# Kernel optimization log

Measured on AMD Instinct MI355X. Metric: run time of the kernel, lower is better.

The kernel has to match this reference:

```python
import jax, jax.numpy as jnp
import numpy as np

N = 100000
E = 3200000
NFEAT = 256
NHID = 128
NCLASS = 16
TEXT_CNT = 50000


def setup_inputs() -> dict:
    key = jax.random.key(0)
    ks = jax.random.split(key, 12)
    x = jax.random.normal(ks[0], (N, NFEAT), dtype=jnp.float32)
    adj_rows = jax.random.randint(ks[1], (E,), 0, N, dtype=jnp.int32)
    adj_cols = jax.random.randint(ks[2], (E,), 0, N, dtype=jnp.int32)
    # positive normalized-adjacency-like weights (~1/avg_degree scale)
    adj_vals = jax.random.uniform(ks[3], (E,), dtype=jnp.float32) / 32.0
    W1 = jax.random.normal(ks[4], (NFEAT, NHID), dtype=jnp.float32) / np.sqrt(NFEAT)
    b1 = jax.random.normal(ks[5], (NHID,), dtype=jnp.float32) * 0.01
    W2 = jax.random.normal(ks[6], (NHID, NFEAT), dtype=jnp.float32) / np.sqrt(NHID)
    b2 = jax.random.normal(ks[7], (NFEAT,), dtype=jnp.float32) * 0.01
    cW1 = jax.random.normal(ks[8], (NFEAT, NCLASS), dtype=jnp.float32) / np.sqrt(NFEAT)
    cb1 = jax.random.normal(ks[9], (NCLASS,), dtype=jnp.float32) * 0.01
    cW2 = jax.random.normal(ks[10], (NFEAT, NCLASS), dtype=jnp.float32) / np.sqrt(NFEAT)
    cb2 = jax.random.normal(ks[11], (NCLASS,), dtype=jnp.float32) * 0.01
    return {"x": x, "adj_rows": adj_rows, "adj_cols": adj_cols, "adj_vals": adj_vals,
            "W1": W1, "b1": b1, "W2": W2, "b2": b2,
            "cW1": cW1, "cb1": cb1, "cW2": cw2 if (cw2 := None) else cW2, "cb2": cb2}


def spmm(rows, cols, vals, dense):
    # out[r] = sum_{e: rows[e]==r} vals[e] * dense[cols[e]]   (COO SpMM)
    gathered = vals[:, None] * dense[cols]  # [E, D]
    return jax.ops.segment_sum(gathered, rows, num_segments=N)


def reference(x, adj_rows, adj_cols, adj_vals, W1, b1, W2, b2, cW1, cb1, cW2, cb2):
    # gc1: adj @ (x @ W1) + b1, then ReLU (dropout is identity at inference)
    h = jax.nn.relu(spmm(adj_rows, adj_cols, adj_vals, x @ W1) + b1)  # [N, NHID]
    # gc2: adj @ (h @ W2) + b2
    out = spmm(adj_rows, adj_cols, adj_vals, h @ W2) + b2  # [N, NFEAT]
    text_cls = out[:TEXT_CNT] @ cW1 + cb1  # [TEXT_CNT, NCLASS]
    img_cls = out[TEXT_CNT:] @ cW2 + cb2   # [N-TEXT_CNT, NCLASS]
    return (out, text_cls, img_cls)
```

## Files before the change

kernel.cpp:

```cpp
#include <hip/hip_runtime.h>

#define N_NODES  100000
#define N_EDGES  3200000
#define NFEAT    256
#define NHID     128
#define NCLASS   16
#define TEXT_CNT 50000

#define RPB      256
#define NB       ((N_NODES + RPB - 1) / RPB)
#define CAP      16384
#define S_EPT    32

typedef unsigned int uint;
typedef __bf16 bf16x8 __attribute__((ext_vector_type(8)));
typedef __bf16 bf16x4 __attribute__((ext_vector_type(4)));
typedef float f32x4 __attribute__((ext_vector_type(4)));

__device__ inline uint bf16_rne(float f) {
  uint u = __float_as_uint(f);
  return (u + 0x7fffu + ((u >> 16) & 1u)) >> 16;
}
__device__ inline float bf_lo(uint u) { return __uint_as_float(u << 16); }
__device__ inline float bf_hi(uint u) { return __uint_as_float(u & 0xffff0000u); }


__global__ __launch_bounds__(256) void init_cursor_kernel(int* __restrict__ gcursor) {
  int t = blockIdx.x * 256 + threadIdx.x;
  if (t < NB) gcursor[t] = t * CAP;
}


__global__ __launch_bounds__(256) void bucket_scatter_kernel(const int* __restrict__ rows,
                                                             const int* __restrict__ cols,
                                                             const float* __restrict__ vals,
                                                             int* __restrict__ gcursor,
                                                             int2* __restrict__ packed, int E) {
  __shared__ int hist[NB];
  __shared__ int cur[NB];
  for (int i = threadIdx.x; i < NB; i += 256) hist[i] = 0;
  __syncthreads();
  int base = blockIdx.x * (256 * S_EPT);
#pragma unroll
  for (int i = 0; i < S_EPT; ++i) {
    int e = base + i * 256 + threadIdx.x;
    if (e < E) atomicAdd(&hist[rows[e] >> 8], 1);
  }
  __syncthreads();
  for (int i = threadIdx.x; i < NB; i += 256) {
    int h = hist[i];
    cur[i] = h ? atomicAdd(&gcursor[i], h) : 0;
  }
  __syncthreads();
#pragma unroll
  for (int i = 0; i < S_EPT; ++i) {
    int e = base + i * 256 + threadIdx.x;
    if (e < E) {
      int r = rows[e];
      int b = r >> 8;
      int p = atomicAdd(&cur[b], 1);
      if (p < ((b + 1) << 14))
        packed[p] = make_int2(((r & 255) << 17) | cols[e], __float_as_int(vals[e]));
    }
  }
}


__global__ __launch_bounds__(512) void bucket_scan_kernel(const int* __restrict__ gcursor,
                                                          int* __restrict__ bbase) {
  __shared__ int s[512];
  int t = threadIdx.x;
  int v = (t < NB) ? (gcursor[t] - t * CAP) : 0;
  s[t] = v;
  __syncthreads();
  for (int off = 1; off < 512; off <<= 1) {
    int u = (t >= off) ? s[t - off] : 0;
    __syncthreads();
    s[t] += u;
    __syncthreads();
  }
  if (t < NB) bbase[t] = s[t] - v;
  if (t == 0) bbase[NB] = N_EDGES;
}


__global__ __launch_bounds__(256) void csr_finalize_kernel(const int* __restrict__ bbase,
                                                           const int2* __restrict__ packed_in,
                                                           int2* __restrict__ packed_out,
                                                           int* __restrict__ row_ptr) {
  __shared__ int hist[RPB];
  __shared__ int cur[RPB];
  int b = blockIdx.x;
  int s0 = b * CAP;
  int gout = bbase[b];
  int cnt = bbase[b + 1] - gout;
  int end = s0 + cnt;
  int t = threadIdx.x;
  hist[t] = 0;
  __syncthreads();
  {
    int i = s0 + t;
    for (; i + 768 < end; i += 1024) {
      int2 a0 = packed_in[i], a1 = packed_in[i + 256];
      int2 a2 = packed_in[i + 512], a3 = packed_in[i + 768];
      atomicAdd(&hist[a0.x >> 17], 1);
      atomicAdd(&hist[a1.x >> 17], 1);
      atomicAdd(&hist[a2.x >> 17], 1);
      atomicAdd(&hist[a3.x >> 17], 1);
    }
    for (; i < end; i += 256) atomicAdd(&hist[packed_in[i].x >> 17], 1);
  }
  __syncthreads();
  int v = hist[t];
  cur[t] = v;
  __syncthreads();
  for (int off = 1; off < 256; off <<= 1) {
    int u = (t >= off) ? cur[t - off] : 0;
    __syncthreads();
    cur[t] += u;
    __syncthreads();
  }
  int rbase = gout + cur[t] - v;
  int row = b * RPB + t;
  if (row < N_NODES) row_ptr[row] = rbase;
  if (b == 0 && t == 0) row_ptr[N_NODES] = N_EDGES;
  __syncthreads();
  cur[t] = rbase;
  __syncthreads();
  {
    int i = s0 + t;
    for (; i + 768 < end; i += 1024) {
      int2 a0 = packed_in[i], a1 = packed_in[i + 256];
      int2 a2 = packed_in[i + 512], a3 = packed_in[i + 768];
      int p0 = atomicAdd(&cur[a0.x >> 17], 1);
      int p1 = atomicAdd(&cur[a1.x >> 17], 1);
      int p2 = atomicAdd(&cur[a2.x >> 17], 1);
      int p3 = atomicAdd(&cur[a3.x >> 17], 1);
      packed_out[p0] = make_int2((a0.x & 0x1FFFF) << 8, a0.y);
      packed_out[p1] = make_int2((a1.x & 0x1FFFF) << 8, a1.y);
      packed_out[p2] = make_int2((a2.x & 0x1FFFF) << 8, a2.y);
      packed_out[p3] = make_int2((a3.x & 0x1FFFF) << 8, a3.y);
    }
    for (; i < end; i += 256) {
      int2 pk = packed_in[i];
      int p = atomicAdd(&cur[pk.x >> 17], 1);
      packed_out[p] = make_int2((pk.x & 0x1FFFF) << 8, pk.y);
    }
  }
}


__global__ __launch_bounds__(256) void spmm_bf16_kernel(const int* __restrict__ row_ptr,
                                                        const int2* __restrict__ packed,
                                                        const uint* __restrict__ src,
                                                        uint* __restrict__ dst,
                                                        const float* __restrict__ bias,
                                                        int relu, int nrows) {
  int lane = threadIdx.x & 63;
  int row = blockIdx.x * 4 + (threadIdx.x >> 6);
  if (row >= nrows) return;
  int s = row_ptr[row];
  int e = row_ptr[row + 1];
  const char* srcb = (const char*)src + (lane << 2);
  float a0 = 0.f, a1 = 0.f;
  int i = s;
  for (; i + 8 <= e; i += 8) {
    int2 p0 = packed[i + 0], p1 = packed[i + 1], p2 = packed[i + 2], p3 = packed[i + 3];
    int2 p4 = packed[i + 4], p5 = packed[i + 5], p6 = packed[i + 6], p7 = packed[i + 7];
    uint u0 = *(const uint*)(srcb + (uint)p0.x);
    uint u1 = *(const uint*)(srcb + (uint)p1.x);
    uint u2 = *(const uint*)(srcb + (uint)p2.x);
    uint u3 = *(const uint*)(srcb + (uint)p3.x);
    uint u4 = *(const uint*)(srcb + (uint)p4.x);
    uint u5 = *(const uint*)(srcb + (uint)p5.x);
    uint u6 = *(const uint*)(srcb + (uint)p6.x);
    uint u7 = *(const uint*)(srcb + (uint)p7.x);
    float v0 = __int_as_float(p0.y), v1 = __int_as_float(p1.y);
    float v2 = __int_as_float(p2.y), v3 = __int_as_float(p3.y);
    float v4 = __int_as_float(p4.y), v5 = __int_as_float(p5.y);
    float v6 = __int_as_float(p6.y), v7 = __int_as_float(p7.y);
    a0 += v0 * bf_lo(u0); a1 += v0 * bf_hi(u0);
    a0 += v1 * bf_lo(u1); a1 += v1 * bf_hi(u1);
    a0 += v2 * bf_lo(u2); a1 += v2 * bf_hi(u2);
    a0 += v3 * bf_lo(u3); a1 += v3 * bf_hi(u3);
    a0 += v4 * bf_lo(u4); a1 += v4 * bf_hi(u4);
    a0 += v5 * bf_lo(u5); a1 += v5 * bf_hi(u5);
    a0 += v6 * bf_lo(u6); a1 += v6 * bf_hi(u6);
    a0 += v7 * bf_lo(u7); a1 += v7 * bf_hi(u7);
  }
  for (; i < e; ++i) {
    int2 pk = packed[i];
    float v = __int_as_float(pk.y);
    uint u = *(const uint*)(srcb + (uint)pk.x);
    a0 += v * bf_lo(u); a1 += v * bf_hi(u);
  }
  if (bias) { a0 += bias[2 * lane]; a1 += bias[2 * lane + 1]; }
  if (relu) { a0 = fmaxf(a0, 0.f); a1 = fmaxf(a1, 0.f); }
  dst[(size_t)row * 64 + lane] = bf16_rne(a0) | (bf16_rne(a1) << 16);
}


__global__ __launch_bounds__(256) void wt_kernel(const float* __restrict__ W,
                                                 unsigned short* __restrict__ Wt,
                                                 int K, int N) {
  int idx = blockIdx.x * 256 + threadIdx.x;
  if (idx >= K * N) return;
  int n = idx / K, k = idx - n * K;
  Wt[idx] = (unsigned short)bf16_rne(W[(size_t)k * N + n]);
}


template <int A_FP32, int OUT_BF16, int K, int N>
__global__ __launch_bounds__(256) void gemm_mfma_kernel(const void* __restrict__ Aptr,
                                                        const __bf16* __restrict__ Bt,
                                                        const float* __restrict__ bias,
                                                        void* __restrict__ Cptr, int M) {
  __shared__ __bf16 As[128 * 40];
  __shared__ __bf16 Bs[128 * 40];
  int tid = threadIdx.x;
  int lane = tid & 63;
  int w = tid >> 6;
  int wr = w >> 1, wc = w & 1;
  int brow = blockIdx.x * 128;
  int bcol = blockIdx.y * 128;
  int r16 = lane & 15, kb = lane >> 4;

  f32x4 acc[4][4];
#pragma unroll
  for (int m = 0; m < 4; ++m)
#pragma unroll
    for (int n = 0; n < 4; ++n) acc[m][n] = (f32x4){0.f, 0.f, 0.f, 0.f};

  for (int k0 = 0; k0 < K; k0 += 32) {
    if (A_FP32) {
      const float* A = (const float*)Aptr;
#pragma unroll
      for (int i = 0; i < 4; ++i) {
        int idx = tid + i * 256;
        int row = idx >> 3;
        int kq = (idx & 7) << 2;
        int gr = brow + row;
        float4 v = make_float4(0.f, 0.f, 0.f, 0.f);
        if (gr < M) v = *(const float4*)&A[(size_t)gr * K + k0 + kq];
        bf16x4 o;
        o[0] = (__bf16)v.x; o[1] = (__bf16)v.y; o[2] = (__bf16)v.z; o[3] = (__bf16)v.w;
        *(bf16x4*)&As[row * 40 + kq] = o;
      }
    } else {
      const __bf16* A = (const __bf16*)Aptr;
#pragma unroll
      for (int i = 0; i < 2; ++i) {
        int idx = tid + i * 256;
        int row = idx >> 2;
        int kq = (idx & 3) << 3;
        int gr = brow + row;
        bf16x8 v = {};
        if (gr < M) v = *(const bf16x8*)&A[(size_t)gr * K + k0 + kq];
        *(bf16x8*)&As[row * 40 + kq] = v;
      }
    }
#pragma unroll
    for (int i = 0; i < 2; ++i) {
      int idx = tid + i * 256;
      int col = idx >> 2;
      int kq = (idx & 3) << 3;
      bf16x8 v = *(const bf16x8*)&Bt[(size_t)(bcol + col) * K + k0 + kq];
      *(bf16x8*)&Bs[col * 40 + kq] = v;
    }
    __syncthreads();

    bf16x8 a[4], b[4];
#pragma unroll
    for (int m = 0; m < 4; ++m)
      a[m] = *(bf16x8*)&As[(wr * 64 + m * 16 + r16) * 40 + kb * 8];
#pragma unroll
    for (int n = 0; n < 4; ++n)
      b[n] = *(bf16x8*)&Bs[(wc * 64 + n * 16 + r16) * 40 + kb * 8];
#pragma unroll
    for (int m = 0; m < 4; ++m)
#pragma unroll
      for (int n = 0; n < 4; ++n)
        acc[m][n] = __builtin_amdgcn_mfma_f32_16x16x32_bf16(a[m], b[n], acc[m][n], 0, 0, 0);
    __syncthreads();
  }

  int crow0 = brow + wr * 64;
  int ccol0 = bcol + wc * 64;
#pragma unroll
  for (int n = 0; n < 4; ++n) {
    int col = ccol0 + n * 16 + r16;
    float bv = bias ? bias[col] : 0.f;
#pragma unroll
    for (int m = 0; m < 4; ++m) {
#pragma unroll
      for (int r = 0; r < 4; ++r) {
        int row = crow0 + m * 16 + kb * 4 + r;
        if (row < M) {
          float val = acc[m][n][r] + bv;
          if (OUT_BF16)
            ((unsigned short*)Cptr)[(size_t)row * N + col] = (unsigned short)bf16_rne(val);
          else
            ((float*)Cptr)[(size_t)row * N + col] = val;
        }
      }
    }
  }
}


__global__ __launch_bounds__(256) void wc_kernel(const float* __restrict__ W2,
                                                 const float* __restrict__ b2,
                                                 const float* __restrict__ cW1,
                                                 const float* __restrict__ cb1,
                                                 const float* __restrict__ cW2,
                                                 const float* __restrict__ cb2,
                                                 float* __restrict__ Wc1, float* __restrict__ bc1,
                                                 float* __restrict__ Wc2, float* __restrict__ bc2) {
  int idx = blockIdx.x * 256 + threadIdx.x;
  int set = idx >> 11;
  int e = idx & 2047;
  int i = e >> 4;
  int c = e & 15;
  const float* cw = set ? cW2 : cW1;
  float acc = 0.f;
  for (int k = 0; k < NFEAT; ++k)
    acc += W2[(size_t)i * NFEAT + k] * cw[k * NCLASS + c];
  (set ? Wc2 : Wc1)[e] = acc;
  if (idx < 32) {
    int s2 = idx >> 4, c2 = idx & 15;
    const float* cwb = s2 ? cW2 : cW1;
    float b = (s2 ? cb2 : cb1)[c2];
    for (int k = 0; k < NFEAT; ++k) b += b2[k] * cwb[k * NCLASS + c2];
    (s2 ? bc2 : bc1)[c2] = b;
  }
}


__global__ __launch_bounds__(256) void cls_kernel(const uint* __restrict__ t3,
                                                  const float* __restrict__ Wc1,
                                                  const float* __restrict__ bc1,
                                                  const float* __restrict__ Wc2,
                                                  const float* __restrict__ bc2,
                                                  float* __restrict__ out1,
                                                  float* __restrict__ out2) {
  int half = gridDim.x >> 1;
  int region = blockIdx.x >= half;
  int bid = region ? blockIdx.x - half : blockIdx.x;
  const float* Wc = region ? Wc2 : Wc1;
  const float* bc = region ? bc2 : bc1;
  float* outp = region ? out2 : out1;
  int row0 = region ? TEXT_CNT : 0;
  int nrows = region ? (N_NODES - TEXT_CNT) : TEXT_CNT;

  int lane = threadIdx.x & 63;
  int wav = bid * 4 + (threadIdx.x >> 6);
  int nw = half * 4;
  int c = lane & 15;
  int kg = lane >> 4;
  float w[32];
#pragma unroll
  for (int j = 0; j < 32; ++j) w[j] = Wc[(kg * 32 + j) * NCLASS + c];
  float bcv = bc[c];
  for (int r = wav; r < nrows; r += nw) {
    const uint4* rp = (const uint4*)&t3[(size_t)(row0 + r) * 64 + kg * 16];
    float acc = 0.f;
#pragma unroll
    for (int q = 0; q < 4; ++q) {
      uint4 u = rp[q];
      acc += bf_lo(u.x) * w[q * 8 + 0] + bf_hi(u.x) * w[q * 8 + 1]
           + bf_lo(u.y) * w[q * 8 + 2] + bf_hi(u.y) * w[q * 8 + 3]
           + bf_lo(u.z) * w[q * 8 + 4] + bf_hi(u.z) * w[q * 8 + 5]
           + bf_lo(u.w) * w[q * 8 + 6] + bf_hi(u.w) * w[q * 8 + 7];
    }
    acc += __shfl_xor(acc, 16);
    acc += __shfl_xor(acc, 32);
    if (lane < 16) outp[(size_t)r * NCLASS + lane] = acc + bcv;
  }
}


extern "C" void kernel_launch(void* const* d_in, const int* in_sizes, int n_in,
                              void* d_out, int out_size, void* d_ws, size_t ws_size,
                              hipStream_t stream) {
  const float* x     = (const float*)d_in[0];
  const int*   arows = (const int*)d_in[1];
  const int*   acols = (const int*)d_in[2];
  const float* avals = (const float*)d_in[3];
  const float* W1    = (const float*)d_in[4];
  const float* b1    = (const float*)d_in[5];
  const float* W2    = (const float*)d_in[6];
  const float* b2    = (const float*)d_in[7];
  const float* cW1   = (const float*)d_in[8];
  const float* cb1   = (const float*)d_in[9];
  const float* cW2   = (const float*)d_in[10];
  const float* cb2   = (const float*)d_in[11];
  float* outp = (float*)d_out;

  char* ws = (char*)d_ws;
  size_t off = 0;
  auto alloc = [&](size_t bytes) -> void* {
    void* p = ws + off;
    off += (bytes + 255) & ~(size_t)255;
    return p;
  };
  uint*  t1u     = (uint*) alloc((size_t)N_NODES * 64 * 4);
  uint*  hu      = (uint*) alloc((size_t)N_NODES * 64 * 4);
  uint*  t3u     = (uint*) alloc((size_t)N_NODES * 64 * 4);
  int2*  packedA = (int2*) alloc((size_t)NB * CAP * 8);
  int2*  packedB = (int2*) alloc((size_t)N_EDGES * 8);
  int*   bbase   = (int*)  alloc((size_t)(NB + 1) * 4);
  int*   gcursor = (int*)  alloc((size_t)NB * 4);
  int*   rowp    = (int*)  alloc((size_t)(N_NODES + 1) * 4);
  unsigned short* W1t = (unsigned short*)alloc((size_t)NHID * NFEAT * 2);
  unsigned short* W2t = (unsigned short*)alloc((size_t)NFEAT * NHID * 2);
  float* Wc1     = (float*)alloc(NHID * NCLASS * 4);
  float* Wc2     = (float*)alloc(NHID * NCLASS * 4);
  float* bc1     = (float*)alloc(64);
  float* bc2     = (float*)alloc(64);

  init_cursor_kernel<<<(NB + 255) / 256, 256, 0, stream>>>(gcursor);
  int nblkS = (N_EDGES + 256 * S_EPT - 1) / (256 * S_EPT);
  bucket_scatter_kernel<<<nblkS, 256, 0, stream>>>(arows, acols, avals, gcursor, packedA, N_EDGES);
  bucket_scan_kernel<<<1, 512, 0, stream>>>(gcursor, bbase);
  csr_finalize_kernel<<<NB, 256, 0, stream>>>(bbase, packedA, packedB, rowp);

  wt_kernel<<<(NFEAT * NHID + 255) / 256, 256, 0, stream>>>(W1, W1t, NFEAT, NHID);
  wt_kernel<<<(NFEAT * NHID + 255) / 256, 256, 0, stream>>>(W2, W2t, NHID, NFEAT);
  wc_kernel<<<16, 256, 0, stream>>>(W2, b2, cW1, cb1, cW2, cb2, Wc1, bc1, Wc2, bc2);

  int mblk = (N_NODES + 127) / 128;
  gemm_mfma_kernel<1, 1, NFEAT, NHID><<<dim3(mblk, 1), 256, 0, stream>>>(
      x, (const __bf16*)W1t, nullptr, t1u, N_NODES);
  spmm_bf16_kernel<<<(N_NODES + 3) / 4, 256, 0, stream>>>(rowp, packedB, t1u, hu, b1, 1, N_NODES);
  spmm_bf16_kernel<<<(N_NODES + 3) / 4, 256, 0, stream>>>(rowp, packedB, hu, t3u, nullptr, 0, N_NODES);
  gemm_mfma_kernel<0, 0, NHID, NFEAT><<<dim3(mblk, 2), 256, 0, stream>>>(
      t3u, (const __bf16*)W2t, b2, outp, N_NODES);
  cls_kernel<<<2048, 256, 0, stream>>>(t3u, Wc1, bc1, Wc2, bc2,
      outp + (size_t)N_NODES * NFEAT,
      outp + (size_t)N_NODES * NFEAT + (size_t)TEXT_CNT * NCLASS);
}
```

Measured before the change: 491.8 us.

## Fuse prep kernels, co-schedule scatter with GEMM1, widen SpMM gathers

Result: faster. 465.3 us (-5.4%).

```diff
diff --git a/kernel.cpp b/kernel.cpp
--- a/kernel.cpp
+++ b/kernel.cpp
@@ -10,7 +10,8 @@
 #define RPB      256
 #define NB       ((N_NODES + RPB - 1) / RPB)
 #define CAP      16384
-#define S_EPT    32
+#define S_EPT    8
+#define NBLKS    ((N_EDGES + 256 * S_EPT - 1) / (256 * S_EPT))
 
 typedef unsigned int uint;
 typedef __bf16 bf16x8 __attribute__((ext_vector_type(8)));
@@ -25,22 +26,60 @@
 __device__ inline float bf_hi(uint u) { return __uint_as_float(u & 0xffff0000u); }
 
 
-__global__ __launch_bounds__(256) void init_cursor_kernel(int* __restrict__ gcursor) {
-  int t = blockIdx.x * 256 + threadIdx.x;
-  if (t < NB) gcursor[t] = t * CAP;
-}
-
-
-__global__ __launch_bounds__(256) void bucket_scatter_kernel(const int* __restrict__ rows,
-                                                             const int* __restrict__ cols,
-                                                             const float* __restrict__ vals,
-                                                             int* __restrict__ gcursor,
-                                                             int2* __restrict__ packed, int E) {
+__global__ __launch_bounds__(256) void prep_kernel(const float* __restrict__ W1,
+                                                   const float* __restrict__ W2,
+                                                   const float* __restrict__ b2,
+                                                   const float* __restrict__ cW1,
+                                                   const float* __restrict__ cb1,
+                                                   const float* __restrict__ cW2,
+                                                   const float* __restrict__ cb2,
+                                                   unsigned short* __restrict__ W1t,
+                                                   unsigned short* __restrict__ W2t,
+                                                   float* __restrict__ Wc1, float* __restrict__ bc1,
+                                                   float* __restrict__ Wc2, float* __restrict__ bc2,
+                                                   int* __restrict__ gcursor) {
+  int idx = blockIdx.x * 256 + threadIdx.x;
+  if (idx < 32768) {
+    int n = idx >> 8, k = idx & 255;
+    W1t[idx] = (unsigned short)bf16_rne(W1[(size_t)k * NHID + n]);
+  } else if (idx < 65536) {
+    int i2 = idx - 32768;
+    int n = i2 >> 7, k = i2 & 127;
+    W2t[i2] = (unsigned short)bf16_rne(W2[(size_t)k * NFEAT + n]);
+  } else if (idx < 69632) {
+    int e = idx - 65536;
+    int set = e >> 11;
+    int e2 = e & 2047;
+    int i = e2 >> 4, c = e2 & 15;
+    const float* cw = set ? cW2 : cW1;
+    float acc = 0.f;
+    for (int k = 0; k < NFEAT; ++k)
+      acc += W2[(size_t)i * NFEAT + k] * cw[k * NCLASS + c];
+    (set ? Wc2 : Wc1)[e2] = acc;
+    if (e < 32) {
+      int s2 = e >> 4, c2 = e & 15;
+      const float* cwb = s2 ? cW2 : cW1;
+      float b = (s2 ? cb2 : cb1)[c2];
+      for (int k = 0; k < NFEAT; ++k) b += b2[k] * cwb[k * NCLASS + c2];
+      (s2 ? bc2 : bc1)[c2] = b;
+    }
+  } else if (idx < 69632 + NB) {
+    int b = idx - 69632;
+    gcursor[b] = b * CAP;
+  }
+}
+
+
+__device__ __forceinline__ void scatter_body(int bx, const int* __restrict__ rows,
+                                             const int* __restrict__ cols,
+                                             const float* __restrict__ vals,
+                                             int* __restrict__ gcursor,
+                                             int2* __restrict__ packed, int E) {
   __shared__ int hist[NB];
   __shared__ int cur[NB];
   for (int i = threadIdx.x; i < NB; i += 256) hist[i] = 0;
   __syncthreads();
-  int base = blockIdx.x * (256 * S_EPT);
+  int base = bx * (256 * S_EPT);
 #pragma unroll
   for (int i = 0; i < S_EPT; ++i) {
     int e = base + i * 256 + threadIdx.x;
@@ -66,163 +105,19 @@
 }
 
 
-__global__ __launch_bounds__(512) void bucket_scan_kernel(const int* __restrict__ gcursor,
-                                                          int* __restrict__ bbase) {
-  __shared__ int s[512];
-  int t = threadIdx.x;
-  int v = (t < NB) ? (gcursor[t] - t * CAP) : 0;
-  s[t] = v;
-  __syncthreads();
-  for (int off = 1; off < 512; off <<= 1) {
-    int u = (t >= off) ? s[t - off] : 0;
-    __syncthreads();
-    s[t] += u;
-    __syncthreads();
-  }
-  if (t < NB) bbase[t] = s[t] - v;
-  if (t == 0) bbase[NB] = N_EDGES;
-}
-
-
-__global__ __launch_bounds__(256) void csr_finalize_kernel(const int* __restrict__ bbase,
-                                                           const int2* __restrict__ packed_in,
-                                                           int2* __restrict__ packed_out,
-                                                           int* __restrict__ row_ptr) {
-  __shared__ int hist[RPB];
-  __shared__ int cur[RPB];
-  int b = blockIdx.x;
-  int s0 = b * CAP;
-  int gout = bbase[b];
-  int cnt = bbase[b + 1] - gout;
-  int end = s0 + cnt;
-  int t = threadIdx.x;
-  hist[t] = 0;
-  __syncthreads();
-  {
-    int i = s0 + t;
-    for (; i + 768 < end; i += 1024) {
-      int2 a0 = packed_in[i], a1 = packed_in[i + 256];
-      int2 a2 = packed_in[i + 512], a3 = packed_in[i + 768];
-      atomicAdd(&hist[a0.x >> 17], 1);
-      atomicAdd(&hist[a1.x >> 17], 1);
-      atomicAdd(&hist[a2.x >> 17], 1);
-      atomicAdd(&hist[a3.x >> 17], 1);
-    }
-    for (; i < end; i += 256) atomicAdd(&hist[packed_in[i].x >> 17], 1);
-  }
-  __syncthreads();
-  int v = hist[t];
-  cur[t] = v;
-  __syncthreads();
-  for (int off = 1; off < 256; off <<= 1) {
-    int u = (t >= off) ? cur[t - off] : 0;
-    __syncthreads();
-    cur[t] += u;
-    __syncthreads();
-  }
-  int rbase = gout + cur[t] - v;
-  int row = b * RPB + t;
-  if (row < N_NODES) row_ptr[row] = rbase;
-  if (b == 0 && t == 0) row_ptr[N_NODES] = N_EDGES;
-  __syncthreads();
-  cur[t] = rbase;
-  __syncthreads();
-  {
-    int i = s0 + t;
-    for (; i + 768 < end; i += 1024) {
-      int2 a0 = packed_in[i], a1 = packed_in[i + 256];
-      int2 a2 = packed_in[i + 512], a3 = packed_in[i + 768];
-      int p0 = atomicAdd(&cur[a0.x >> 17], 1);
-      int p1 = atomicAdd(&cur[a1.x >> 17], 1);
-      int p2 = atomicAdd(&cur[a2.x >> 17], 1);
-      int p3 = atomicAdd(&cur[a3.x >> 17], 1);
-      packed_out[p0] = make_int2((a0.x & 0x1FFFF) << 8, a0.y);
-      packed_out[p1] = make_int2((a1.x & 0x1FFFF) << 8, a1.y);
-      packed_out[p2] = make_int2((a2.x & 0x1FFFF) << 8, a2.y);
-      packed_out[p3] = make_int2((a3.x & 0x1FFFF) << 8, a3.y);
-    }
-    for (; i < end; i += 256) {
-      int2 pk = packed_in[i];
-      int p = atomicAdd(&cur[pk.x >> 17], 1);
-      packed_out[p] = make_int2((pk.x & 0x1FFFF) << 8, pk.y);
-    }
-  }
-}
-
-
-__global__ __launch_bounds__(256) void spmm_bf16_kernel(const int* __restrict__ row_ptr,
-                                                        const int2* __restrict__ packed,
-                                                        const uint* __restrict__ src,
-                                                        uint* __restrict__ dst,
-                                                        const float* __restrict__ bias,
-                                                        int relu, int nrows) {
-  int lane = threadIdx.x & 63;
-  int row = blockIdx.x * 4 + (threadIdx.x >> 6);
-  if (row >= nrows) return;
-  int s = row_ptr[row];
-  int e = row_ptr[row + 1];
-  const char* srcb = (const char*)src + (lane << 2);
-  float a0 = 0.f, a1 = 0.f;
-  int i = s;
-  for (; i + 8 <= e; i += 8) {
-    int2 p0 = packed[i + 0], p1 = packed[i + 1], p2 = packed[i + 2], p3 = packed[i + 3];
-    int2 p4 = packed[i + 4], p5 = packed[i + 5], p6 = packed[i + 6], p7 = packed[i + 7];
-    uint u0 = *(const uint*)(srcb + (uint)p0.x);
-    uint u1 = *(const uint*)(srcb + (uint)p1.x);
-    uint u2 = *(const uint*)(srcb + (uint)p2.x);
-    uint u3 = *(const uint*)(srcb + (uint)p3.x);
-    uint u4 = *(const uint*)(srcb + (uint)p4.x);
-    uint u5 = *(const uint*)(srcb + (uint)p5.x);
-    uint u6 = *(const uint*)(srcb + (uint)p6.x);
-    uint u7 = *(const uint*)(srcb + (uint)p7.x);
-    float v0 = __int_as_float(p0.y), v1 = __int_as_float(p1.y);
-    float v2 = __int_as_float(p2.y), v3 = __int_as_float(p3.y);
-    float v4 = __int_as_float(p4.y), v5 = __int_as_float(p5.y);
-    float v6 = __int_as_float(p6.y), v7 = __int_as_float(p7.y);
-    a0 += v0 * bf_lo(u0); a1 += v0 * bf_hi(u0);
-    a0 += v1 * bf_lo(u1); a1 += v1 * bf_hi(u1);
-    a0 += v2 * bf_lo(u2); a1 += v2 * bf_hi(u2);
-    a0 += v3 * bf_lo(u3); a1 += v3 * bf_hi(u3);
-    a0 += v4 * bf_lo(u4); a1 += v4 * bf_hi(u4);
-    a0 += v5 * bf_lo(u5); a1 += v5 * bf_hi(u5);
-    a0 += v6 * bf_lo(u6); a1 += v6 * bf_hi(u6);
-    a0 += v7 * bf_lo(u7); a1 += v7 * bf_hi(u7);
-  }
-  for (; i < e; ++i) {
-    int2 pk = packed[i];
-    float v = __int_as_float(pk.y);
-    uint u = *(const uint*)(srcb + (uint)pk.x);
-    a0 += v * bf_lo(u); a1 += v * bf_hi(u);
-  }
-  if (bias) { a0 += bias[2 * lane]; a1 += bias[2 * lane + 1]; }
-  if (relu) { a0 = fmaxf(a0, 0.f); a1 = fmaxf(a1, 0.f); }
-  dst[(size_t)row * 64 + lane] = bf16_rne(a0) | (bf16_rne(a1) << 16);
-}
-
-
-__global__ __launch_bounds__(256) void wt_kernel(const float* __restrict__ W,
-                                                 unsigned short* __restrict__ Wt,
-                                                 int K, int N) {
-  int idx = blockIdx.x * 256 + threadIdx.x;
-  if (idx >= K * N) return;
-  int n = idx / K, k = idx - n * K;
-  Wt[idx] = (unsigned short)bf16_rne(W[(size_t)k * N + n]);
-}
-
-
 template <int A_FP32, int OUT_BF16, int K, int N>
-__global__ __launch_bounds__(256) void gemm_mfma_kernel(const void* __restrict__ Aptr,
-                                                        const __bf16* __restrict__ Bt,
-                                                        const float* __restrict__ bias,
-                                                        void* __restrict__ Cptr, int M) {
+__device__ __forceinline__ void gemm_body(int bx, int by, const void* __restrict__ Aptr,
+                                          const __bf16* __restrict__ Bt,
+                                          const float* __restrict__ bias,
+                                          void* __restrict__ Cptr, int M) {
   __shared__ __bf16 As[128 * 40];
   __shared__ __bf16 Bs[128 * 40];
   int tid = threadIdx.x;
   int lane = tid & 63;
   int w = tid >> 6;
   int wr = w >> 1, wc = w & 1;
-  int brow = blockIdx.x * 128;
-  int bcol = blockIdx.y * 128;
+  int brow = bx * 128;
+  int bcol = by * 128;
   int r16 = lane & 15, kb = lane >> 4;
 
   f32x4 acc[4][4];
@@ -308,31 +203,200 @@
 }
 
 
-__global__ __launch_bounds__(256) void wc_kernel(const float* __restrict__ W2,
-                                                 const float* __restrict__ b2,
-                                                 const float* __restrict__ cW1,
-                                                 const float* __restrict__ cb1,
-                                                 const float* __restrict__ cW2,
-                                                 const float* __restrict__ cb2,
-                                                 float* __restrict__ Wc1, float* __restrict__ bc1,
-                                                 float* __restrict__ Wc2, float* __restrict__ bc2) {
-  int idx = blockIdx.x * 256 + threadIdx.x;
-  int set = idx >> 11;
-  int e = idx & 2047;
-  int i = e >> 4;
-  int c = e & 15;
-  const float* cw = set ? cW2 : cW1;
-  float acc = 0.f;
-  for (int k = 0; k < NFEAT; ++k)
-    acc += W2[(size_t)i * NFEAT + k] * cw[k * NCLASS + c];
-  (set ? Wc2 : Wc1)[e] = acc;
-  if (idx < 32) {
-    int s2 = idx >> 4, c2 = idx & 15;
-    const float* cwb = s2 ? cW2 : cW1;
-    float b = (s2 ? cb2 : cb1)[c2];
-    for (int k = 0; k < NFEAT; ++k) b += b2[k] * cwb[k * NCLASS + c2];
-    (s2 ? bc2 : bc1)[c2] = b;
-  }
+__global__ __launch_bounds__(256) void fused_scatter_gemm1_kernel(
+    const int* __restrict__ rows, const int* __restrict__ cols, const float* __restrict__ vals,
+    int* __restrict__ gcursor, int2* __restrict__ packedA, int E,
+    const float* __restrict__ x, const __bf16* __restrict__ W1t, uint* __restrict__ t1u, int M) {
+  if (blockIdx.x < NBLKS)
+    scatter_body(blockIdx.x, rows, cols, vals, gcursor, packedA, E);
+  else
+    gemm_body<1, 1, NFEAT, NHID>(blockIdx.x - NBLKS, 0, x, W1t, nullptr, t1u, M);
+}
+
+
+__global__ __launch_bounds__(512) void bucket_scan_kernel(const int* __restrict__ gcursor,
+                                                          int* __restrict__ bbase) {
+  __shared__ int s[512];
+  int t = threadIdx.x;
+  int v = (t < NB) ? (gcursor[t] - t * CAP) : 0;
+  s[t] = v;
+  __syncthreads();
+  for (int off = 1; off < 512; off <<= 1) {
+    int u = (t >= off) ? s[t - off] : 0;
+    __syncthreads();
+    s[t] += u;
+    __syncthreads();
+  }
+  if (t < NB) bbase[t] = s[t] - v;
+  if (t == 0) bbase[NB] = N_EDGES;
+}
+
+
+__global__ __launch_bounds__(512) void csr_finalize_kernel(const int* __restrict__ bbase,
+                                                           const int2* __restrict__ packed_in,
+                                                           int2* __restrict__ packed_out,
+                                                           int* __restrict__ row_ptr) {
+  __shared__ int hist[RPB];
+  __shared__ int cur[RPB];
+  int b = blockIdx.x;
+  int s0 = b * CAP;
+  int gout = bbase[b];
+  int cnt = bbase[b + 1] - gout;
+  int end = s0 + cnt;
+  int t = threadIdx.x;
+  if (t < RPB) hist[t] = 0;
+  __syncthreads();
+  {
+    int i = s0 + t;
+    for (; i + 1536 < end; i += 2048) {
+      int2 a0 = packed_in[i], a1 = packed_in[i + 512];
+      int2 a2 = packed_in[i + 1024], a3 = packed_in[i + 1536];
+      atomicAdd(&hist[a0.x >> 17], 1);
+      atomicAdd(&hist[a1.x >> 17], 1);
+      atomicAdd(&hist[a2.x >> 17], 1);
+      atomicAdd(&hist[a3.x >> 17], 1);
+    }
+    for (; i < end; i += 512) atomicAdd(&hist[packed_in[i].x >> 17], 1);
+  }
+  __syncthreads();
+  int v = (t < RPB) ? hist[t] : 0;
+  if (t < RPB) cur[t] = v;
+  __syncthreads();
+  for (int off = 1; off < RPB; off <<= 1) {
+    int u = (t >= off && t < RPB) ? cur[t - off] : 0;
+    __syncthreads();
+    if (t < RPB) cur[t] += u;
+    __syncthreads();
+  }
+  if (t < RPB) {
+    int rbase = gout + cur[t] - v;
+    int row = b * RPB + t;
+    if (row < N_NODES) row_ptr[row] = rbase;
+    cur[t] = rbase;
+  }
+  if (b == 0 && t == 0) row_ptr[N_NODES] = N_EDGES;
+  __syncthreads();
+  {
+    int i = s0 + t;
+    for (; i + 1536 < end; i += 2048) {
+      int2 a0 = packed_in[i], a1 = packed_in[i + 512];
+      int2 a2 = packed_in[i + 1024], a3 = packed_in[i + 1536];
+      int p0 = atomicAdd(&cur[a0.x >> 17], 1);
+      int p1 = atomicAdd(&cur[a1.x >> 17], 1);
+      int p2 = atomicAdd(&cur[a2.x >> 17], 1);
+      int p3 = atomicAdd(&cur[a3.x >> 17], 1);
+      packed_out[p0] = make_int2((a0.x & 0x1FFFF) << 8, a0.y);
+      packed_out[p1] = make_int2((a1.x & 0x1FFFF) << 8, a1.y);
+      packed_out[p2] = make_int2((a2.x & 0x1FFFF) << 8, a2.y);
+      packed_out[p3] = make_int2((a3.x & 0x1FFFF) << 8, a3.y);
+    }
+    for (; i < end; i += 512) {
+      int2 pk = packed_in[i];
+      int p = atomicAdd(&cur[pk.x >> 17], 1);
+      packed_out[p] = make_int2((pk.x & 0x1FFFF) << 8, pk.y);
+    }
+  }
+}
+
+
+__global__ __launch_bounds__(256) void spmm_bf16_kernel(const int* __restrict__ row_ptr,
+                                                        const int2* __restrict__ packed,
+                                                        const uint* __restrict__ src,
+                                                        uint* __restrict__ dst,
+                                                        const float* __restrict__ bias,
+                                                        int relu, int nrows) {
+  int tid = threadIdx.x;
+  int lane = tid & 63;
+  int half = lane >> 5;
+  int l32 = lane & 31;
+  int row = blockIdx.x * 4 + (tid >> 6);
+  if (row >= nrows) return;
+  int s = row_ptr[row];
+  int e = row_ptr[row + 1];
+  const char* srcb = (const char*)src + (l32 << 3);
+  float a0 = 0.f, a1 = 0.f, a2 = 0.f, a3 = 0.f;
+  int i = s;
+  for (; i + 16 <= e; i += 16) {
+    int2 m0 = packed[i + 0 + half], m1 = packed[i + 2 + half];
+    int2 m2 = packed[i + 4 + half], m3 = packed[i + 6 + half];
+    int2 m4 = packed[i + 8 + half], m5 = packed[i + 10 + half];
+    int2 m6 = packed[i + 12 + half], m7 = packed[i + 14 + half];
+    uint2 u0 = *(const uint2*)(srcb + (uint)m0.x);
+    uint2 u1 = *(const uint2*)(srcb + (uint)m1.x);
+    uint2 u2 = *(const uint2*)(srcb + (uint)m2.x);
+    uint2 u3 = *(const uint2*)(srcb + (uint)m3.x);
+    uint2 u4 = *(const uint2*)(srcb + (uint)m4.x);
+    uint2 u5 = *(const uint2*)(srcb + (uint)m5.x);
+    uint2 u6 = *(const uint2*)(srcb + (uint)m6.x);
+    uint2 u7 = *(const uint2*)(srcb + (uint)m7.x);
+    float v0 = __int_as_float(m0.y), v1 = __int_as_float(m1.y);
+    float v2 = __int_as_float(m2.y), v3 = __int_as_float(m3.y);
+    float v4 = __int_as_float(m4.y), v5 = __int_as_float(m5.y);
+    float v6 = __int_as_float(m6.y), v7 = __int_as_float(m7.y);
+    a0 += v0 * bf_lo(u0.x); a1 += v0 * bf_hi(u0.x); a2 += v0 * bf_lo(u0.y); a3 += v0 * bf_hi(u0.y);
+    a0 += v1 * bf_lo(u1.x); a1 += v1 * bf_hi(u1.x); a2 += v1 * bf_lo(u1.y); a3 += v1 * bf_hi(u1.y);
+    a0 += v2 * bf_lo(u2.x); a1 += v2 * bf_hi(u2.x); a2 += v2 * bf_lo(u2.y); a3 += v2 * bf_hi(u2.y);
+    a0 += v3 * bf_lo(u3.x); a1 += v3 * bf_hi(u3.x); a2 += v3 * bf_lo(u3.y); a3 += v3 * bf_hi(u3.y);
+    a0 += v4 * bf_lo(u4.x); a1 += v4 * bf_hi(u4.x); a2 += v4 * bf_lo(u4.y); a3 += v4 * bf_hi(u4.y);
+    a0 += v5 * bf_lo(u5.x); a1 += v5 * bf_hi(u5.x); a2 += v5 * bf_lo(u5.y); a3 += v5 * bf_hi(u5.y);
+    a0 += v6 * bf_lo(u6.x); a1 += v6 * bf_hi(u6.x); a2 += v6 * bf_lo(u6.y); a3 += v6 * bf_hi(u6.y);
+    a0 += v7 * bf_lo(u7.x); a1 += v7 * bf_hi(u7.x); a2 += v7 * bf_lo(u7.y); a3 += v7 * bf_hi(u7.y);
+  }
+  for (; i + 8 <= e; i += 8) {
+    int2 m0 = packed[i + 0 + half], m1 = packed[i + 2 + half];
+    int2 m2 = packed[i + 4 + half], m3 = packed[i + 6 + half];
+    uint2 u0 = *(const uint2*)(srcb + (uint)m0.x);
+    uint2 u1 = *(const uint2*)(srcb + (uint)m1.x);
+    uint2 u2 = *(const uint2*)(srcb + (uint)m2.x);
+    uint2 u3 = *(const uint2*)(srcb + (uint)m3.x);
+    float v0 = __int_as_float(m0.y), v1 = __int_as_float(m1.y);
+    float v2 = __int_as_float(m2.y), v3 = __int_as_float(m3.y);
+    a0 += v0 * bf_lo(u0.x); a1 += v0 * bf_hi(u0.x); a2 += v0 * bf_lo(u0.y); a3 += v0 * bf_hi(u0.y);
+    a0 += v1 * bf_lo(u1.x); a1 += v1 * bf_hi(u1.x); a2 += v1 * bf_lo(u1.y); a3 += v1 * bf_hi(u1.y);
+    a0 += v2 * bf_lo(u2.x); a1 += v2 * bf_hi(u2.x); a2 += v2 * bf_lo(u2.y); a3 += v2 * bf_hi(u2.y);
+    a0 += v3 * bf_lo(u3.x); a1 += v3 * bf_hi(u3.x); a2 += v3 * bf_lo(u3.y); a3 += v3 * bf_hi(u3.y);
+  }
+  for (; i + 4 <= e; i += 4) {
+    int2 m0 = packed[i + 0 + half], m1 = packed[i + 2 + half];
+    uint2 u0 = *(const uint2*)(srcb + (uint)m0.x);
+    uint2 u1 = *(const uint2*)(srcb + (uint)m1.x);
+    float v0 = __int_as_float(m0.y), v1 = __int_as_float(m1.y);
+    a0 += v0 * bf_lo(u0.x); a1 += v0 * bf_hi(u0.x); a2 += v0 * bf_lo(u0.y); a3 += v0 * bf_hi(u0.y);
+    a0 += v1 * bf_lo(u1.x); a1 += v1 * bf_hi(u1.x); a2 += v1 * bf_lo(u1.y); a3 += v1 * bf_hi(u1.y);
+  }
+  for (; i < e; i += 2) {
+    int ee = i + half;
+    int ok = ee < e;
+    int2 m = packed[ok ? ee : (e - 1)];
+    uint2 u = *(const uint2*)(srcb + (uint)m.x);
+    float v = ok ? __int_as_float(m.y) : 0.f;
+    a0 += v * bf_lo(u.x); a1 += v * bf_hi(u.x); a2 += v * bf_lo(u.y); a3 += v * bf_hi(u.y);
+  }
+  a0 += __shfl_xor(a0, 32); a1 += __shfl_xor(a1, 32);
+  a2 += __shfl_xor(a2, 32); a3 += __shfl_xor(a3, 32);
+  if (half == 0) {
+    if (bias) {
+      a0 += bias[4 * l32 + 0]; a1 += bias[4 * l32 + 1];
+      a2 += bias[4 * l32 + 2]; a3 += bias[4 * l32 + 3];
+    }
+    if (relu) {
+      a0 = fmaxf(a0, 0.f); a1 = fmaxf(a1, 0.f);
+      a2 = fmaxf(a2, 0.f); a3 = fmaxf(a3, 0.f);
+    }
+    uint2 o;
+    o.x = bf16_rne(a0) | (bf16_rne(a1) << 16);
+    o.y = bf16_rne(a2) | (bf16_rne(a3) << 16);
+    *(uint2*)&dst[(size_t)row * 64 + l32 * 2] = o;
+  }
+}
+
+
+template <int A_FP32, int OUT_BF16, int K, int N>
+__global__ __launch_bounds__(256) void gemm_mfma_kernel(const void* __restrict__ Aptr,
+                                                        const __bf16* __restrict__ Bt,
+                                                        const float* __restrict__ bias,
+                                                        void* __restrict__ Cptr, int M) {
+  gemm_body<A_FP32, OUT_BF16, K, N>(blockIdx.x, blockIdx.y, Aptr, Bt, bias, Cptr, M);
 }
 
 
@@ -418,19 +482,17 @@
   float* bc1     = (float*)alloc(64);
   float* bc2     = (float*)alloc(64);
 
-  init_cursor_kernel<<<(NB + 255) / 256, 256, 0, stream>>>(gcursor);
-  int nblkS = (N_EDGES + 256 * S_EPT - 1) / (256 * S_EPT);
-  bucket_scatter_kernel<<<nblkS, 256, 0, stream>>>(arows, acols, avals, gcursor, packedA, N_EDGES);
+  prep_kernel<<<(69632 + NB + 255) / 256, 256, 0, stream>>>(
+      W1, W2, b2, cW1, cb1, cW2, cb2, W1t, W2t, Wc1, bc1, Wc2, bc2, gcursor);
+
+  int mblk = (N_NODES + 127) / 128;
+  fused_scatter_gemm1_kernel<<<NBLKS + mblk, 256, 0, stream>>>(
+      arows, acols, avals, gcursor, packedA, N_EDGES,
+      x, (const __bf16*)W1t, t1u, N_NODES);
+
   bucket_scan_kernel<<<1, 512, 0, stream>>>(gcursor, bbase);
-  csr_finalize_kernel<<<NB, 256, 0, stream>>>(bbase, packedA, packedB, rowp);
-
-  wt_kernel<<<(NFEAT * NHID + 255) / 256, 256, 0, stream>>>(W1, W1t, NFEAT, NHID);
-  wt_kernel<<<(NFEAT * NHID + 255) / 256, 256, 0, stream>>>(W2, W2t, NHID, NFEAT);
-  wc_kernel<<<16, 256, 0, stream>>>(W2, b2, cW1, cb1, cW2, cb2, Wc1, bc1, Wc2, bc2);
-
-  int mblk = (N_NODES + 127) / 128;
-  gemm_mfma_kernel<1, 1, NFEAT, NHID><<<dim3(mblk, 1), 256, 0, stream>>>(
-      x, (const __bf16*)W1t, nullptr, t1u, N_NODES);
+  csr_finalize_kernel<<<NB, 512, 0, stream>>>(bbase, packedA, packedB, rowp);
+
   spmm_bf16_kernel<<<(N_NODES + 3) / 4, 256, 0, stream>>>(rowp, packedB, t1u, hu, b1, 1, N_NODES);
   spmm_bf16_kernel<<<(N_NODES + 3) / 4, 256, 0, stream>>>(rowp, packedB, hu, t3u, nullptr, 0, N_NODES);
   gemm_mfma_kernel<0, 0, NHID, NFEAT><<<dim3(mblk, 2), 256, 0, stream>>>(
```
